# Kernel tuning notes

Hardware: AMD Instinct MI355X
Metric: run time of the kernel (lower is better)

Reference implementation:

```python
import jax, jax.numpy as jnp
import numpy as np

HIDDEN = 768
HEADS = 12
HEAD_DIM = HIDDEN // HEADS
GRID_SIZE = 5
SPLINE_ORDER = 3
COEFF = GRID_SIZE + SPLINE_ORDER  # 8
ROPE_THETA = 10000.0


def _make_grid():
    # uniform grid over [-1, 1] extended by spline_order knots on each side
    h = 2.0 / GRID_SIZE
    return jnp.arange(-SPLINE_ORDER, GRID_SIZE + SPLINE_ORDER + 1, dtype=jnp.float32) * h - 1.0


def _b_splines(x2d, grid):
    # x2d: (N, in) -> bases: (N, in, COEFF) via Cox-de Boor recursion
    xg = x2d[..., None]  # (N, in, 1)
    bases = ((xg >= grid[:-1]) & (xg < grid[1:])).astype(x2d.dtype)
    for k in range(1, SPLINE_ORDER + 1):
        left = (xg - grid[: -(k + 1)]) / (grid[k:-1] - grid[: -(k + 1)]) * bases[..., :-1]
        right = (grid[k + 1:] - xg) / (grid[k + 1:] - grid[1:-k]) * bases[..., 1:]
        bases = left + right
    return bases


def _kan_linear(x, base_w, spline_w, scaler, grid):
    # x: (..., in); base_w: (out, in); spline_w: (out, in, COEFF); scaler: (out, in)
    orig = x.shape
    x2d = x.reshape(-1, orig[-1])
    base = jax.nn.silu(x2d) @ base_w.T
    bases = _b_splines(x2d, grid)                       # (N, in, COEFF)
    scaled_w = spline_w * scaler[..., None]             # (out, in, COEFF)
    spline = jnp.einsum('nic,oic->no', bases, scaled_w)
    return (base + spline).reshape(*orig[:-1], -1)


def _rope(q, k):
    # q, k: (B, H, S, D); GPT-NeoX style rotate_half RoPE
    S, D = q.shape[-2], q.shape[-1]
    inv_freq = 1.0 / (ROPE_THETA ** (jnp.arange(0, D, 2, dtype=jnp.float32) / D))
    t = jnp.arange(S, dtype=jnp.float32)
    freqs = jnp.outer(t, inv_freq)                      # (S, D/2)
    emb = jnp.concatenate([freqs, freqs], axis=-1)      # (S, D)
    cos, sin = jnp.cos(emb), jnp.sin(emb)

    def rot_half(u):
        u1, u2 = u[..., : D // 2], u[..., D // 2:]
        return jnp.concatenate([-u2, u1], axis=-1)

    q = q * cos + rot_half(q) * sin
    k = k * cos + rot_half(k) * sin
    return q, k


def setup_inputs() -> dict:
    key = jax.random.key(0)
    ks = jax.random.split(key, 12)
    s_base = 1.0 / np.sqrt(HIDDEN)
    s_spline = 0.1 / np.sqrt(HIDDEN)
    d = {
        'x': jax.random.normal(ks[0], (4, 1024, HIDDEN), jnp.float32) * 0.5,
        'q_base_w': jax.random.normal(ks[1], (HIDDEN, HIDDEN), jnp.float32) * s_base,
        'q_spline_w': jax.random.normal(ks[2], (HIDDEN, HIDDEN, COEFF), jnp.float32) * s_spline,
        'q_scaler': 1.0 + 0.1 * jax.random.normal(ks[3], (HIDDEN, HIDDEN), jnp.float32),
        'k_base_w': jax.random.normal(ks[4], (HIDDEN, HIDDEN), jnp.float32) * s_base,
        'k_spline_w': jax.random.normal(ks[5], (HIDDEN, HIDDEN, COEFF), jnp.float32) * s_spline,
        'k_scaler': 1.0 + 0.1 * jax.random.normal(ks[6], (HIDDEN, HIDDEN), jnp.float32),
        'v_base_w': jax.random.normal(ks[7], (HIDDEN, HIDDEN), jnp.float32) * s_base,
        'v_spline_w': jax.random.normal(ks[8], (HIDDEN, HIDDEN, COEFF), jnp.float32) * s_spline,
        'v_scaler': 1.0 + 0.1 * jax.random.normal(ks[9], (HIDDEN, HIDDEN), jnp.float32),
        'out_w': jax.random.normal(ks[10], (HIDDEN, HIDDEN), jnp.float32) * s_base,
        'out_b': jnp.zeros((HIDDEN,), jnp.float32),
    }
    return d


def reference(x, q_base_w, q_spline_w, q_scaler, k_base_w, k_spline_w, k_scaler,
              v_base_w, v_spline_w, v_scaler, out_w, out_b):
    B, S, _ = x.shape
    grid = _make_grid()
    q = _kan_linear(x, q_base_w, q_spline_w, q_scaler, grid)
    k = _kan_linear(x, k_base_w, k_spline_w, k_scaler, grid)
    v = _kan_linear(x, v_base_w, v_spline_w, v_scaler, grid)
    # (B, S, H, D) -> (B, H, S, D)
    q = q.reshape(B, S, HEADS, HEAD_DIM).transpose(0, 2, 1, 3)
    k = k.reshape(B, S, HEADS, HEAD_DIM).transpose(0, 2, 1, 3)
    v = v.reshape(B, S, HEADS, HEAD_DIM).transpose(0, 2, 1, 3)
    q, k = _rope(q, k)
    scores = jnp.einsum('bhqd,bhkd->bhqk', q, k) / jnp.sqrt(jnp.float32(HEAD_DIM))
    alphas = jax.nn.softmax(scores, axis=-1)
    attn = jnp.einsum('bhqk,bhkd->bhqd', alphas, v)
    attn = attn.transpose(0, 2, 1, 3).reshape(B, S, HIDDEN)
    return attn @ out_w.T + out_b
```

## Files before the change

### kernel.cpp

```cpp
#include <hip/hip_runtime.h>
#include <hip/hip_bf16.h>
#include <hip/hip_fp16.h>

#define HIDDEN 768
#define NTOK   4096
#define SEQ    1024
#define NBATCH 4
#define NHEADS 12
#define KAUG   (HIDDEN * 9)
#define NQKV   (3 * HIDDEN)

using bf16 = __hip_bfloat16;
using fp16 = __half;
typedef __attribute__((ext_vector_type(4))) float f32x4;
typedef __attribute__((ext_vector_type(8))) short bf16x8;
typedef __attribute__((ext_vector_type(8))) _Float16 h16x8;

__device__ inline void gload_lds16(const void* g, void* l) {
    __builtin_amdgcn_global_load_lds((const __attribute__((address_space(1))) void*)g,
                                     (__attribute__((address_space(3))) void*)l, 16, 0, 0);
}

__global__ __launch_bounds__(256) void prep(const float* __restrict__ x,
        const float* __restrict__ qbw, const float* __restrict__ qsw, const float* __restrict__ qsc,
        const float* __restrict__ kbw, const float* __restrict__ ksw, const float* __restrict__ ksc,
        const float* __restrict__ vbw, const float* __restrict__ vsw, const float* __restrict__ vsc,
        bf16* __restrict__ xa, bf16* __restrict__ wa) {
    int blk = blockIdx.x;
    const int tid = threadIdx.x;
    if (blk < 12288) {
        int gid = blk * 256 + tid;
        float xv = x[gid];
        int n = gid / HIDDEN;
        int i = gid - n * HIDDEN;
        float sil = xv / (1.0f + __expf(-xv));
        float g[12];
#pragma unroll
        for (int k = 0; k < 12; ++k) g[k] = (float)(k - 3) * 0.4f - 1.0f;
        float b[11];
#pragma unroll
        for (int c = 0; c < 11; ++c) b[c] = (xv >= g[c] && xv < g[c + 1]) ? 1.0f : 0.0f;
#pragma unroll
        for (int k = 1; k <= 3; ++k) {
#pragma unroll
            for (int c = 0; c < 11; ++c) {
                if (c < 11 - k) {
                    float left  = (xv - g[c]) / (g[c + k] - g[c]) * b[c];
                    float right = (g[c + k + 1] - xv) / (g[c + k + 1] - g[c + 1]) * b[c + 1];
                    b[c] = left + right;
                }
            }
        }
        bf16* row = xa + (size_t)n * KAUG;
        row[i] = __float2bfloat16(sil);
        bf16 bb[8];
#pragma unroll
        for (int c = 0; c < 8; ++c) bb[c] = __float2bfloat16(b[c]);
        *(bf16x8*)&row[768 + i * 8] = *(bf16x8*)bb;
        return;
    }
    blk -= 12288;
    int job = blk / 2304;
    int gid = (blk - job * 2304) * 256 + tid;
    const float* bw = job == 0 ? qbw : (job == 1 ? kbw : vbw);
    const float* sw = job == 0 ? qsw : (job == 1 ? ksw : vsw);
    const float* sc = job == 0 ? qsc : (job == 1 ? ksc : vsc);
    int o = gid / HIDDEN;
    int i = gid - o * HIDDEN;
    float bwv = bw[gid];
    float scv = sc[gid];
    bf16* row = wa + (size_t)job * HIDDEN * KAUG + (size_t)o * KAUG;
    row[i] = __float2bfloat16(bwv);
    bf16 ss[8];
#pragma unroll
    for (int c = 0; c < 8; ++c) ss[c] = __float2bfloat16(sw[(size_t)gid * 8 + c] * scv);
    *(bf16x8*)&row[768 + i * 8] = *(bf16x8*)ss;
}

template <int KSPLIT>
__global__ __launch_bounds__(512, 2) void gemm256_8ph(const bf16* __restrict__ A,
                                                      const bf16* __restrict__ B,
                                                      fp16* __restrict__ C,
                                                      int M, int N, int K) {
    extern __shared__ char smem[];
    const int tid  = threadIdx.x;
    const int lane = tid & 63;
    const int wave = tid >> 6;
    const int wm = wave >> 2;
    const int wn = wave & 3;

    int lin = blockIdx.y * gridDim.x + blockIdx.x;
    int row0, col0;
    if (gridDim.x == 16 && gridDim.y == 9) {
        int xcd = lin & 7;
        int idx = lin >> 3;
        int rsel = (idx >= 9) ? 1 : 0;
        row0 = (xcd * 2 + rsel) * 256;
        col0 = (idx - rsel * 9) * 256;
    } else {
        const int nwg = gridDim.x * gridDim.y;
        const int per = nwg >> 3;
        int swz = (lin & 7) * per + (lin >> 3);
        row0 = (swz % gridDim.x) * 256;
        col0 = (swz / gridDim.x) * 256;
    }

    const int kslice = K / KSPLIT;
    const int koff = blockIdx.z * kslice;
    const int ntiles = kslice >> 6;
    fp16* Cs = C + (size_t)blockIdx.z * M * N;

    const int lr = lane & 15;
    const int lk = (lane >> 4) * 8;
    const int xorv = (lr & 7) << 4;

    f32x4 acc[8][4];
#pragma unroll
    for (int m = 0; m < 8; ++m)
#pragma unroll
        for (int n = 0; n < 4; ++n) acc[m][n] = f32x4{0.f, 0.f, 0.f, 0.f};

    auto stage_half = [&](int buf, int half, int t) {
#pragma unroll
        for (int j = 0; j < 2; ++j) {
            int idx = tid + j * 512;
            int r = idx >> 3;
            int swzc = ((((idx & 7) * 16) ^ ((r & 7) << 4)) >> 1);
            const bf16* src = (half < 2)
                ? A + (size_t)(row0 + half * 128 + r) * K + koff + t * 64 + swzc
                : B + (size_t)(col0 + (half - 2) * 128 + r) * K + koff + t * 64 + swzc;
            gload_lds16(src, smem + ((size_t)(buf * 4 + half) << 14) + idx * 16);
        }
    };
    auto rdA = [&](int buf, int mh, bf16x8 (&af)[4][2]) {
        const char* Ab = smem + ((size_t)(buf * 4 + wm) << 14);
#pragma unroll
        for (int m = 0; m < 4; ++m)
#pragma unroll
            for (int kk = 0; kk < 2; ++kk)
                af[m][kk] = *(const bf16x8*)(Ab + (mh * 64 + m * 16 + lr) * 128 +
                                             (((kk * 32 + lk) * 2) ^ xorv));
    };
    auto rdB = [&](int buf, int nh, bf16x8 (&bf)[2][2]) {
        const char* Bb = smem + ((size_t)(buf * 4 + 2 + (wn >> 1)) << 14);
#pragma unroll
        for (int n = 0; n < 2; ++n)
#pragma unroll
            for (int kk = 0; kk < 2; ++kk)
                bf[n][kk] = *(const bf16x8*)(Bb + ((wn & 1) * 64 + nh * 32 + n * 16 + lr) * 128 +
                                             (((kk * 32 + lk) * 2) ^ xorv));
    };

    stage_half(0, 0, 0); stage_half(0, 1, 0); stage_half(0, 2, 0); stage_half(0, 3, 0);
    stage_half(1, 2, 1); stage_half(1, 3, 1);
    asm volatile("s_waitcnt vmcnt(0)" ::: "memory");
    __builtin_amdgcn_s_barrier();

    bf16x8 af[4][2], bf0[2][2], bf1[2][2];

#define QUAD(MH, NH, BF)                                                         \
    __builtin_amdgcn_s_setprio(1);                                               \
    _Pragma("unroll") for (int m = 0; m < 4; ++m)                                \
        _Pragma("unroll") for (int n = 0; n < 2; ++n)                            \
            _Pragma("unroll") for (int kk = 0; kk < 2; ++kk)                     \
                acc[(MH)*4 + m][(NH)*2 + n] = __builtin_amdgcn_mfma_f32_16x16x32_bf16( \
                    af[m][kk], BF[n][kk], acc[(MH)*4 + m][(NH)*2 + n], 0, 0, 0); \
    __builtin_amdgcn_s_setprio(0);

    for (int u = 0; u < ntiles; ++u) {
        const int buf = u & 1, nbuf = buf ^ 1;
        rdA(buf, 0, af);
        rdB(buf, 0, bf0);
        if (u + 1 < ntiles) stage_half(nbuf, 0, u + 1);
        __builtin_amdgcn_s_barrier();
        asm volatile("s_waitcnt lgkmcnt(0)" ::: "memory");
        __builtin_amdgcn_sched_barrier(0);
        QUAD(0, 0, bf0)
        __builtin_amdgcn_sched_barrier(0);
        __builtin_amdgcn_s_barrier();
        rdB(buf, 1, bf1);
        if (u + 1 < ntiles) stage_half(nbuf, 1, u + 1);
        __builtin_amdgcn_s_barrier();
        asm volatile("s_waitcnt lgkmcnt(0)" ::: "memory");
        __builtin_amdgcn_sched_barrier(0);
        QUAD(0, 1, bf1)
        __builtin_amdgcn_sched_barrier(0);
        __builtin_amdgcn_s_barrier();
        rdA(buf, 1, af);
        if (u + 2 < ntiles) stage_half(buf, 2, u + 2);
        __builtin_amdgcn_s_barrier();
        asm volatile("s_waitcnt lgkmcnt(0)" ::: "memory");
        __builtin_amdgcn_sched_barrier(0);
        QUAD(1, 1, bf1)
        __builtin_amdgcn_sched_barrier(0);
        __builtin_amdgcn_s_barrier();
        if (u + 2 < ntiles) {
            stage_half(buf, 3, u + 2);
            asm volatile("s_waitcnt vmcnt(4)" ::: "memory");
        } else {
            asm volatile("s_waitcnt vmcnt(0)" ::: "memory");
        }
        __builtin_amdgcn_s_barrier();
        __builtin_amdgcn_sched_barrier(0);
        QUAD(1, 0, bf0)
        __builtin_amdgcn_sched_barrier(0);
        __builtin_amdgcn_s_barrier();
    }
#undef QUAD

    const int cr = (lane >> 4) * 4;
    const int cc = lane & 15;
#pragma unroll
    for (int am = 0; am < 8; ++am) {
#pragma unroll
        for (int an = 0; an < 4; ++an) {
            int c = col0 + wn * 64 + an * 16 + cc;
#pragma unroll
            for (int j = 0; j < 4; ++j) {
                int r = row0 + wm * 128 + am * 16 + cr + j;
                Cs[(size_t)r * N + c] = __float2half(acc[am][an][j]);
            }
        }
    }
}

__global__ __launch_bounds__(256) void gemm_bt(const bf16* __restrict__ A,
                                               const bf16* __restrict__ B,
                                               float* __restrict__ C,
                                               const float* __restrict__ bias,
                                               int M, int N, int K) {
    __shared__ __align__(16) bf16 As[2][128][64];
    __shared__ __align__(16) bf16 Bs[2][128][64];
    const int tid  = threadIdx.x;
    const int lane = tid & 63;
    const int wave = tid >> 6;
    const int wr = wave >> 1, wc = wave & 1;

    const int gx = gridDim.x;
    const int per = (gx * gridDim.y) >> 3;
    int lin = blockIdx.y * gx + blockIdx.x;
    int swz = (lin & 7) * per + (lin >> 3);
    const int row0 = (swz % gx) * 128;
    const int col0 = (swz / gx) * 128;

    f32x4 acc[4][4];
#pragma unroll
    for (int m = 0; m < 4; ++m)
#pragma unroll
        for (int n = 0; n < 4; ++n) acc[m][n] = f32x4{0.f, 0.f, 0.f, 0.f};

    const int srow = tid >> 3;
    const int scol = ((((tid & 7) * 16) ^ ((srow & 7) << 4)) >> 1);
    const bf16* aptr = A + (size_t)(row0 + srow) * K + scol;
    const bf16* bptr = B + (size_t)(col0 + srow) * K + scol;

    const int lr = lane & 15;
    const int lk = (lane >> 4) * 8;
    const int xorv = (lr & 7) << 4;
    const int nt = K >> 6;

    auto stage = [&](int buf, int k0) {
        char* adst = (char*)&As[buf][0][0] + tid * 16;
        char* bdst = (char*)&Bs[buf][0][0] + tid * 16;
#pragma unroll
        for (int j = 0; j < 4; ++j)
            gload_lds16(aptr + (size_t)j * 32 * K + k0, adst + j * 4096);
#pragma unroll
        for (int j = 0; j < 4; ++j)
            gload_lds16(bptr + (size_t)j * 32 * K + k0, bdst + j * 4096);
    };

    stage(0, 0);
    asm volatile("s_waitcnt vmcnt(0)" ::: "memory");
    __syncthreads();

    int cur = 0;
    for (int t = 0; t < nt; ++t) {
        if (t + 1 < nt) stage(cur ^ 1, (t + 1) << 6);
        __builtin_amdgcn_s_setprio(1);
#pragma unroll
        for (int kk = 0; kk < 64; kk += 32) {
            const int cb = ((kk + lk) * 2) ^ xorv;
            bf16x8 af[4], bfv[4];
#pragma unroll
            for (int m = 0; m < 4; ++m)
                af[m] = *(const bf16x8*)((char*)&As[cur][0][0] + (wr * 64 + m * 16 + lr) * 128 + cb);
#pragma unroll
            for (int n = 0; n < 4; ++n)
                bfv[n] = *(const bf16x8*)((char*)&Bs[cur][0][0] + (wc * 64 + n * 16 + lr) * 128 + cb);
#pragma unroll
            for (int m = 0; m < 4; ++m)
#pragma unroll
                for (int n = 0; n < 4; ++n)
                    acc[m][n] = __builtin_amdgcn_mfma_f32_16x16x32_bf16(af[m], bfv[n], acc[m][n], 0, 0, 0);
        }
        __builtin_amdgcn_s_setprio(0);
        __builtin_amdgcn_sched_barrier(0);
        if (t + 1 < nt)
            asm volatile("s_waitcnt vmcnt(0)" ::: "memory");
        __builtin_amdgcn_s_barrier();
        __builtin_amdgcn_sched_barrier(0);
        cur ^= 1;
    }

    const int cr = (lane >> 4) * 4;
    const int cc = lane & 15;
#pragma unroll
    for (int m = 0; m < 4; ++m) {
#pragma unroll
        for (int n = 0; n < 4; ++n) {
            int c = col0 + wc * 64 + n * 16 + cc;
            float bv = bias ? bias[c] : 0.0f;
#pragma unroll
            for (int j = 0; j < 4; ++j) {
                int r = row0 + wr * 64 + m * 16 + cr + j;
                C[(size_t)r * N + c] = acc[m][n][j] + bv;
            }
        }
    }
}

__global__ __launch_bounds__(256) void rope_vt(const fp16* __restrict__ qkv0,
                                               bf16* __restrict__ qb,
                                               bf16* __restrict__ kb,
                                               bf16* __restrict__ vbT,
                                               const float* __restrict__ ow,
                                               bf16* __restrict__ owb) {
    __shared__ bf16 tile[64][65];
    const fp16* qkv1 = qkv0 + (size_t)NTOK * NQKV;
    const fp16* qkv2 = qkv1 + (size_t)NTOK * NQKV;
    int blk = blockIdx.x;
    const int tid = threadIdx.x;
    if (blk < 6144) {
        int gid = blk * 256 + tid;
        int d = gid & 31;
        int h = (gid >> 5) % NHEADS;
        int n = gid / (32 * NHEADS);
        int s = n & (SEQ - 1);
        int b = n >> 10;
        float inv = __expf(-(float)d * 0.28782313662425574f);
        float th = (float)s * inv;
        float sn, cs;
        sincosf(th, &sn, &cs);
        size_t src = (size_t)n * NQKV + h * 64 + d;
        auto rd = [&](size_t idx) {
            return __half2float(qkv0[idx]) + __half2float(qkv1[idx]) + __half2float(qkv2[idx]);
        };
        float q0 = rd(src),       q1 = rd(src + 32);
        float k0 = rd(src + 768), k1 = rd(src + 800);
        int bh = b * NHEADS + h;
        size_t dst = ((size_t)bh * SEQ + s) * 64 + d;
        const float QS = 0.18033688011f;
        qb[dst]      = __float2bfloat16((q0 * cs - q1 * sn) * QS);
        qb[dst + 32] = __float2bfloat16((q1 * cs + q0 * sn) * QS);
        kb[dst]      = __float2bfloat16(k0 * cs - k1 * sn);
        kb[dst + 32] = __float2bfloat16(k1 * cs + k0 * sn);
        return;
    }
    blk -= 6144;
    if (blk < 768) {
        int bh = blk >> 4, st = blk & 15;
        int b = bh / NHEADS, h = bh - b * NHEADS;
        {
            int s = tid >> 2, d0 = (tid & 3) * 16;
            size_t src = (size_t)(b * SEQ + st * 64 + s) * NQKV + 1536 + h * 64 + d0;
#pragma unroll
            for (int c = 0; c < 2; ++c) {
                h16x8 a0 = *(const h16x8*)(qkv0 + src + c * 8);
                h16x8 a1 = *(const h16x8*)(qkv1 + src + c * 8);
                h16x8 a2 = *(const h16x8*)(qkv2 + src + c * 8);
#pragma unroll
                for (int j = 0; j < 8; ++j)
                    tile[s][d0 + c * 8 + j] =
                        __float2bfloat16((float)a0[j] + (float)a1[j] + (float)a2[j]);
            }
        }
        __syncthreads();
        {
            int d = tid >> 2, s0 = (tid & 3) * 16;
            bf16 out[16];
#pragma unroll
            for (int i = 0; i < 16; ++i) out[i] = tile[s0 + i][d];
            bf16* dst = vbT + ((size_t)bh * 64 + d) * SEQ + st * 64 + s0;
            *(bf16x8*)(dst)     = *(bf16x8*)&out[0];
            *(bf16x8*)(dst + 8) = *(bf16x8*)&out[8];
        }
        return;
    }
    blk -= 768;
    int gid = blk * 256 + tid;
    owb[gid] = __float2bfloat16(ow[gid]);
}

__global__ __launch_bounds__(256, 4) void attn_mfma(const bf16* __restrict__ qb,
                                                    const bf16* __restrict__ kb,
                                                    const bf16* __restrict__ vbT,
                                                    bf16* __restrict__ attnb) {
    __shared__ __align__(16) bf16 Kls[64][64];
    __shared__ __align__(16) bf16 Vt[64][64];
    __shared__ __align__(16) bf16 Pls[4][16][72];

    const int tid  = threadIdx.x;
    const int lane = tid & 63;
    const int w    = tid >> 6;
    const int bh   = blockIdx.x;
    const int b    = bh / NHEADS, h = bh - b * NHEADS;
    const int qt   = blockIdx.y;

    const bf16* qhead  = qb  + (size_t)bh * SEQ * 64;
    const char* khead  = (const char*)(kb  + (size_t)bh * SEQ * 64);
    const char* vheadT = (const char*)(vbT + (size_t)bh * 64 * SEQ);

    const int lr = lane & 15;
    const int lg = lane >> 4;
    const int xorv = (lr & 7) << 4;

    const int r0 = tid >> 3;
    const int r1 = (tid + 256) >> 3;
    const int sw0 = ((tid & 7) * 16) ^ ((r0 & 7) << 4);
    const int sw1 = ((tid & 7) * 16) ^ ((r1 & 7) << 4);

    bf16x8 qf[2];
    {
        const bf16* qrow = qhead + (size_t)(qt * 64 + w * 16 + lr) * 64 + lg * 8;
        qf[0] = *(const bf16x8*)qrow;
        qf[1] = *(const bf16x8*)(qrow + 32);
    }

    f32x4 oacc[4];
#pragma unroll
    for (int n = 0; n < 4; ++n) oacc[n] = f32x4{0.f, 0.f, 0.f, 0.f};
    float mrun[4], lsum[4];
#pragma unroll
    for (int j = 0; j < 4; ++j) { mrun[j] = -3.0e38f; lsum[j] = 0.0f; }

    bf16x8 kst0, kst1, vst0, vst1;
    auto load_regs = [&](int t) {
        kst0 = *(const bf16x8*)(khead + (size_t)(t * 64 + r0) * 128 + sw0);
        kst1 = *(const bf16x8*)(khead + (size_t)(t * 64 + r1) * 128 + sw1);
        vst0 = *(const bf16x8*)(vheadT + (size_t)r0 * (SEQ * 2) + t * 128 + sw0);
        vst1 = *(const bf16x8*)(vheadT + (size_t)r1 * (SEQ * 2) + t * 128 + sw1);
    };
    auto write_lds = [&]() {
        *(bf16x8*)((char*)&Kls[0][0] + tid * 16)         = kst0;
        *(bf16x8*)((char*)&Kls[0][0] + (tid + 256) * 16) = kst1;
        *(bf16x8*)((char*)&Vt[0][0] + tid * 16)          = vst0;
        *(bf16x8*)((char*)&Vt[0][0] + (tid + 256) * 16)  = vst1;
    };

    load_regs(0);
    asm volatile("s_waitcnt vmcnt(0)" ::: "memory");
    write_lds();
    asm volatile("s_waitcnt lgkmcnt(0)" ::: "memory");
    __builtin_amdgcn_s_barrier();

    for (int t = 0; t < SEQ / 64; ++t) {
        if (t + 1 < SEQ / 64) load_regs(t + 1);

        f32x4 sacc[4];
#pragma unroll
        for (int n = 0; n < 4; ++n) sacc[n] = f32x4{0.f, 0.f, 0.f, 0.f};
        __builtin_amdgcn_s_setprio(1);
#pragma unroll
        for (int c = 0; c < 2; ++c)
#pragma unroll
            for (int n = 0; n < 4; ++n) {
                bf16x8 kf = *(const bf16x8*)((char*)&Kls[0][0] +
                                             (n * 16 + lr) * 128 + (((c * 32 + lg * 8) * 2) ^ xorv));
                sacc[n] = __builtin_amdgcn_mfma_f32_16x16x32_bf16(qf[c], kf, sacc[n], 0, 0, 0);
            }
        __builtin_amdgcn_s_setprio(0);

        float rowmax[4];
        bool viol = false;
#pragma unroll
        for (int j = 0; j < 4; ++j) {
            rowmax[j] = fmaxf(fmaxf(sacc[0][j], sacc[1][j]), fmaxf(sacc[2][j], sacc[3][j]));
            viol |= rowmax[j] > mrun[j] + 11.5f;
        }
        if (__ballot(viol) != 0ull) {
#pragma unroll
            for (int j = 0; j < 4; ++j) {
                float mx = rowmax[j];
                mx = fmaxf(mx, __shfl_xor(mx, 1));
                mx = fmaxf(mx, __shfl_xor(mx, 2));
                mx = fmaxf(mx, __shfl_xor(mx, 4));
                mx = fmaxf(mx, __shfl_xor(mx, 8));
                float mnew = fmaxf(mrun[j], mx);
                float csc = exp2f(mrun[j] - mnew);
                mrun[j] = mnew;
                lsum[j] *= csc;
#pragma unroll
                for (int n = 0; n < 4; ++n) oacc[n][j] *= csc;
            }
        }

        float pj[4][4];
#pragma unroll
        for (int j = 0; j < 4; ++j) {
            float p0 = exp2f(sacc[0][j] - mrun[j]);
            float p1 = exp2f(sacc[1][j] - mrun[j]);
            float p2 = exp2f(sacc[2][j] - mrun[j]);
            float p3 = exp2f(sacc[3][j] - mrun[j]);
            pj[0][j] = p0; pj[1][j] = p1; pj[2][j] = p2; pj[3][j] = p3;
            lsum[j] += (p0 + p1) + (p2 + p3);
        }

#pragma unroll
        for (int n = 0; n < 4; ++n)
#pragma unroll
            for (int j = 0; j < 4; ++j)
                Pls[w][lg * 4 + j][n * 16 + lr] = __float2bfloat16(pj[n][j]);

        __builtin_amdgcn_s_setprio(1);
#pragma unroll
        for (int c = 0; c < 2; ++c) {
            bf16x8 pf = *(const bf16x8*)&Pls[w][lr][c * 32 + lg * 8];
#pragma unroll
            for (int n = 0; n < 4; ++n) {
                bf16x8 vf = *(const bf16x8*)((char*)&Vt[0][0] +
                                             (n * 16 + lr) * 128 + (((c * 32 + lg * 8) * 2) ^ xorv));
                oacc[n] = __builtin_amdgcn_mfma_f32_16x16x32_bf16(pf, vf, oacc[n], 0, 0, 0);
            }
        }
        __builtin_amdgcn_s_setprio(0);

        if (t + 1 < SEQ / 64) {
            __builtin_amdgcn_s_barrier();
            asm volatile("s_waitcnt vmcnt(0)" ::: "memory");
            write_lds();
            asm volatile("s_waitcnt lgkmcnt(0)" ::: "memory");
            __builtin_amdgcn_s_barrier();
        }
    }

#pragma unroll
    for (int j = 0; j < 4; ++j) {
        float l = lsum[j];
        l += __shfl_xor(l, 1);
        l += __shfl_xor(l, 2);
        l += __shfl_xor(l, 4);
        l += __shfl_xor(l, 8);
        float invl = 1.0f / l;
        int tok = b * SEQ + qt * 64 + w * 16 + lg * 4 + j;
        bf16* dst = attnb + (size_t)tok * HIDDEN + h * 64;
#pragma unroll
        for (int n = 0; n < 4; ++n)
            dst[n * 16 + lr] = __float2bfloat16(oacc[n][j] * invl);
    }
}

extern "C" void kernel_launch(void* const* d_in, const int* in_sizes, int n_in,
                              void* d_out, int out_size, void* d_ws, size_t ws_size,
                              hipStream_t stream) {
    const float* x   = (const float*)d_in[0];
    const float* qbw = (const float*)d_in[1];
    const float* qsw = (const float*)d_in[2];
    const float* qsc = (const float*)d_in[3];
    const float* kbw = (const float*)d_in[4];
    const float* ksw = (const float*)d_in[5];
    const float* ksc = (const float*)d_in[6];
    const float* vbw = (const float*)d_in[7];
    const float* vsw = (const float*)d_in[8];
    const float* vsc = (const float*)d_in[9];
    const float* ow  = (const float*)d_in[10];
    const float* ob  = (const float*)d_in[11];

    char* ws = (char*)d_ws;
    size_t off = 0;
    bf16*  xaug = (bf16*)(ws + off); off += (size_t)NTOK * KAUG * 2;
    bf16*  waug = (bf16*)(ws + off); off += (size_t)NQKV * KAUG * 2;
    fp16*  qkvp = (fp16*)(ws + off); off += (size_t)3 * NTOK * NQKV * 2;
    if (off > ws_size) return;

    bf16* attnb = xaug;
    bf16* owb   = (bf16*)((char*)xaug + (8u << 20));
    const size_t headsz = (size_t)NTOK * 64 * NHEADS;
    bf16* qb  = waug;
    bf16* kb  = waug + headsz;
    bf16* vbT = waug + 2 * headsz;

    hipFuncSetAttribute(reinterpret_cast<const void*>(gemm256_8ph<3>),
                        hipFuncAttributeMaxDynamicSharedMemorySize, 131072);

    prep<<<12288 + 3 * 2304, 256, 0, stream>>>(
        x, qbw, qsw, qsc, kbw, ksw, ksc, vbw, vsw, vsc, xaug, waug);

    gemm256_8ph<3><<<dim3(NTOK / 256, NQKV / 256, 3), 512, 131072, stream>>>(
        xaug, waug, qkvp, NTOK, NQKV, KAUG);

    rope_vt<<<6144 + 768 + 2304, 256, 0, stream>>>(qkvp, qb, kb, vbT, ow, owb);
    attn_mfma<<<dim3(NBATCH * NHEADS, SEQ / 64), 256, 0, stream>>>(qb, kb, vbT, attnb);
    gemm_bt<<<dim3(NTOK / 128, HIDDEN / 128), 256, 0, stream>>>(attnb, owb, (float*)d_out, ob, NTOK, HIDDEN, HIDDEN);
}
```

Measured before the change: 271.8 us.

## Replace double-buffered direct-to-LDS GEMM pipeline with single-buffer register prefetch

Rewrites the main QKV GEMM mainloop. It drops the double-buffered global_load_lds pipeline with fine-grained barriers and uses one LDS buffer instead. The next tile is prefetched into registers while the MFMAs run on the current tile, then written to LDS between two block syncs. This halves LDS use to 64 KB, but it adds many VGPRs for the staging registers and removes the two-blocks-per-CU launch bound. The added syncs may also expose load latency.

```diff
diff --git a/kernel.cpp b/kernel.cpp
--- a/kernel.cpp
+++ b/kernel.cpp
@@ -78,10 +78,10 @@
 }
 
 template <int KSPLIT>
-__global__ __launch_bounds__(512, 2) void gemm256_8ph(const bf16* __restrict__ A,
-                                                      const bf16* __restrict__ B,
-                                                      fp16* __restrict__ C,
-                                                      int M, int N, int K) {
+__global__ __launch_bounds__(512) void gemm256_1buf(const bf16* __restrict__ A,
+                                                    const bf16* __restrict__ B,
+                                                    fp16* __restrict__ C,
+                                                    int M, int N, int K) {
     extern __shared__ char smem[];
     const int tid  = threadIdx.x;
     const int lane = tid & 63;
@@ -120,20 +120,38 @@
 #pragma unroll
         for (int n = 0; n < 4; ++n) acc[m][n] = f32x4{0.f, 0.f, 0.f, 0.f};
 
-    auto stage_half = [&](int buf, int half, int t) {
-#pragma unroll
-        for (int j = 0; j < 2; ++j) {
-            int idx = tid + j * 512;
-            int r = idx >> 3;
-            int swzc = ((((idx & 7) * 16) ^ ((r & 7) << 4)) >> 1);
-            const bf16* src = (half < 2)
-                ? A + (size_t)(row0 + half * 128 + r) * K + koff + t * 64 + swzc
-                : B + (size_t)(col0 + (half - 2) * 128 + r) * K + koff + t * 64 + swzc;
-            gload_lds16(src, smem + ((size_t)(buf * 4 + half) << 14) + idx * 16);
-        }
-    };
-    auto rdA = [&](int buf, int mh, bf16x8 (&af)[4][2]) {
-        const char* Ab = smem + ((size_t)(buf * 4 + wm) << 14);
+    const bf16* srcbase[4][2];
+    {
+#pragma unroll
+        for (int half = 0; half < 4; ++half)
+#pragma unroll
+            for (int j = 0; j < 2; ++j) {
+                int idx = tid + j * 512;
+                int r = idx >> 3;
+                int swzc = ((((idx & 7) * 16) ^ ((r & 7) << 4)) >> 1);
+                srcbase[half][j] = (half < 2)
+                    ? A + (size_t)(row0 + half * 128 + r) * K + koff + swzc
+                    : B + (size_t)(col0 + (half - 2) * 128 + r) * K + koff + swzc;
+            }
+    }
+    bf16x8 st[4][2];
+    auto load_regs = [&](int t) {
+#pragma unroll
+        for (int half = 0; half < 4; ++half)
+#pragma unroll
+            for (int j = 0; j < 2; ++j)
+                st[half][j] = *(const bf16x8*)(srcbase[half][j] + t * 64);
+    };
+    auto write_lds = [&]() {
+#pragma unroll
+        for (int half = 0; half < 4; ++half)
+#pragma unroll
+            for (int j = 0; j < 2; ++j)
+                *(bf16x8*)(smem + ((size_t)half << 14) + (tid + j * 512) * 16) = st[half][j];
+    };
+
+    auto rdA = [&](int mh, bf16x8 (&af)[4][2]) {
+        const char* Ab = smem + ((size_t)wm << 14);
 #pragma unroll
         for (int m = 0; m < 4; ++m)
 #pragma unroll
@@ -141,8 +159,8 @@
                 af[m][kk] = *(const bf16x8*)(Ab + (mh * 64 + m * 16 + lr) * 128 +
                                              (((kk * 32 + lk) * 2) ^ xorv));
     };
-    auto rdB = [&](int buf, int nh, bf16x8 (&bf)[2][2]) {
-        const char* Bb = smem + ((size_t)(buf * 4 + 2 + (wn >> 1)) << 14);
+    auto rdB = [&](int nh, bf16x8 (&bf)[2][2]) {
+        const char* Bb = smem + ((size_t)(2 + (wn >> 1)) << 14);
 #pragma unroll
         for (int n = 0; n < 2; ++n)
 #pragma unroll
@@ -151,60 +169,39 @@
                                              (((kk * 32 + lk) * 2) ^ xorv));
     };
 
-    stage_half(0, 0, 0); stage_half(0, 1, 0); stage_half(0, 2, 0); stage_half(0, 3, 0);
-    stage_half(1, 2, 1); stage_half(1, 3, 1);
-    asm volatile("s_waitcnt vmcnt(0)" ::: "memory");
-    __builtin_amdgcn_s_barrier();
-
-    bf16x8 af[4][2], bf0[2][2], bf1[2][2];
-
 #define QUAD(MH, NH, BF)                                                         \
-    __builtin_amdgcn_s_setprio(1);                                               \
     _Pragma("unroll") for (int m = 0; m < 4; ++m)                                \
         _Pragma("unroll") for (int n = 0; n < 2; ++n)                            \
             _Pragma("unroll") for (int kk = 0; kk < 2; ++kk)                     \
                 acc[(MH)*4 + m][(NH)*2 + n] = __builtin_amdgcn_mfma_f32_16x16x32_bf16( \
-                    af[m][kk], BF[n][kk], acc[(MH)*4 + m][(NH)*2 + n], 0, 0, 0); \
-    __builtin_amdgcn_s_setprio(0);
+                    af[m][kk], BF[n][kk], acc[(MH)*4 + m][(NH)*2 + n], 0, 0, 0);
+
+    load_regs(0);
+    asm volatile("s_waitcnt vmcnt(0)" ::: "memory");
+    write_lds();
+    __syncthreads();
+
+    bf16x8 af[4][2], bf0[2][2], bf1[2][2];
 
     for (int u = 0; u < ntiles; ++u) {
-        const int buf = u & 1, nbuf = buf ^ 1;
-        rdA(buf, 0, af);
-        rdB(buf, 0, bf0);
-        if (u + 1 < ntiles) stage_half(nbuf, 0, u + 1);
-        __builtin_amdgcn_s_barrier();
-        asm volatile("s_waitcnt lgkmcnt(0)" ::: "memory");
-        __builtin_amdgcn_sched_barrier(0);
+        if (u + 1 < ntiles) load_regs(u + 1);
+
+        __builtin_amdgcn_s_setprio(1);
+        rdA(0, af);
+        rdB(0, bf0);
         QUAD(0, 0, bf0)
-        __builtin_amdgcn_sched_barrier(0);
-        __builtin_amdgcn_s_barrier();
-        rdB(buf, 1, bf1);
-        if (u + 1 < ntiles) stage_half(nbuf, 1, u + 1);
-        __builtin_amdgcn_s_barrier();
-        asm volatile("s_waitcnt lgkmcnt(0)" ::: "memory");
-        __builtin_amdgcn_sched_barrier(0);
+        rdB(1, bf1);
         QUAD(0, 1, bf1)
-        __builtin_amdgcn_sched_barrier(0);
-        __builtin_amdgcn_s_barrier();
-        rdA(buf, 1, af);
-        if (u + 2 < ntiles) stage_half(buf, 2, u + 2);
-        __builtin_amdgcn_s_barrier();
-        asm volatile("s_waitcnt lgkmcnt(0)" ::: "memory");
-        __builtin_amdgcn_sched_barrier(0);
+        rdA(1, af);
         QUAD(1, 1, bf1)
-        __builtin_amdgcn_sched_barrier(0);
-        __builtin_amdgcn_s_barrier();
-        if (u + 2 < ntiles) {
-            stage_half(buf, 3, u + 2);
-            asm volatile("s_waitcnt vmcnt(4)" ::: "memory");
-        } else {
-            asm volatile("s_waitcnt vmcnt(0)" ::: "memory");
-        }
-        __builtin_amdgcn_s_barrier();
-        __builtin_amdgcn_sched_barrier(0);
         QUAD(1, 0, bf0)
-        __builtin_amdgcn_sched_barrier(0);
-        __builtin_amdgcn_s_barrier();
+        __builtin_amdgcn_s_setprio(0);
+
+        if (u + 1 < ntiles) {
+            __syncthreads();
+            write_lds();
+            __syncthreads();
+        }
     }
 #undef QUAD
 
@@ -580,13 +577,10 @@
     bf16* kb  = waug + headsz;
     bf16* vbT = waug + 2 * headsz;
 
-    hipFuncSetAttribute(reinterpret_cast<const void*>(gemm256_8ph<3>),
-                        hipFuncAttributeMaxDynamicSharedMemorySize, 131072);
-
     prep<<<12288 + 3 * 2304, 256, 0, stream>>>(
         x, qbw, qsw, qsc, kbw, ksw, ksc, vbw, vsw, vsc, xaug, waug);
 
-    gemm256_8ph<3><<<dim3(NTOK / 256, NQKV / 256, 3), 512, 131072, stream>>>(
+    gemm256_1buf<3><<<dim3(NTOK / 256, NQKV / 256, 3), 512, 65536, stream>>>(
         xaug, waug, qkvp, NTOK, NQKV, KAUG);
 
     rope_vt<<<6144 + 768 + 2304, 256, 0, stream>>>(qkvp, qb, kb, vbT, ow, owb);
```

New measurement: 273.2 us. Within noise of the previous version (+0.5%).
